# Kernel optimization log

Hardware: AMD Instinct MI355X
Metric: run time of the kernel (lower is better)

Reference implementation:

```python
import jax, jax.numpy as jnp
import numpy as np

NEG_SLOPE = 0.2

def setup_inputs() -> dict:
    key = jax.random.key(0)
    k1, k2, k3, k4 = jax.random.split(key, 4)
    B, N, Fin, H, Fo = 8, 2000, 128, 4, 64
    x = jax.random.normal(k1, (B, N, Fin), dtype=jnp.float32)
    adj = jax.random.randint(k2, (N, N), 0, 2, dtype=jnp.int32)
    W = jax.random.normal(k3, (Fin, H * Fo), dtype=jnp.float32) * (1.0 / np.sqrt(Fin))
    a = jax.random.normal(k4, (H, 2 * Fo), dtype=jnp.float32) * 0.1
    return {"x": x, "adj": adj, "W": W, "a": a}

def reference(x, adj, W, a):
    B, N, _ = x.shape
    H, F2 = a.shape
    Fo = F2 // 2
    h = (x @ W).reshape(B, N, H, Fo)  # [B,N,H,Fo]
    # cat([h_i,h_j])*a summed over 2Fo decomposes into per-node src/dst scores
    a_src, a_dst = a[:, :Fo], a[:, Fo:]
    e_i = jnp.einsum('bnhf,hf->bnh', h, a_src)  # source (query) contribution
    e_j = jnp.einsum('bnhf,hf->bnh', h, a_dst)  # target (key) contribution
    e = jax.nn.leaky_relu(e_i[:, :, None, :] + e_j[:, None, :, :], NEG_SLOPE)  # [B,N,N,H]
    mask = (adj == 0)[None, :, :, None]
    e = jnp.where(mask, -jnp.inf, e)
    alpha = jax.nn.softmax(e, axis=2)  # softmax over neighbors j
    # dropout is identity in eval mode
    out = jnp.einsum('bijh,bjhf->bihf', alpha, h).mean(axis=2)  # [B,N,Fo]
    return out, alpha
```

## Files before the change

kernel.cpp:

```cpp
#include <hip/hip_runtime.h>
#include <math.h>

#define BB 8
#define NN 2000
#define FIN 128
#define HH 4
#define FO 64
#define CC 256

typedef short bf16x8 __attribute__((ext_vector_type(8)));
typedef float f32x4 __attribute__((ext_vector_type(4)));
typedef unsigned long long u64;

__device__ __forceinline__ unsigned short f2bf(float v) {
    union { float f; unsigned u; } x;
    x.f = v;
    unsigned r = x.u + 0x7fffu + ((x.u >> 16) & 1u);
    return (unsigned short)(r >> 16);
}

__global__ __launch_bounds__(256) void k_gemm_xw(const float* __restrict__ x,
                                                 const float* __restrict__ W,
                                                 float* __restrict__ hfeat) {
    __shared__ float xs[16 * FIN];
    const int row0 = blockIdx.x * 16;
    const int t = threadIdx.x;
    for (int k = t; k < 16 * FIN; k += 256) xs[k] = x[row0 * FIN + k];
    __syncthreads();
    const int c = t;
    float acc[16];
#pragma unroll
    for (int r = 0; r < 16; ++r) acc[r] = 0.f;
#pragma unroll 2
    for (int k = 0; k < FIN; k += 4) {
        const float w0 = W[(k + 0) * CC + c];
        const float w1 = W[(k + 1) * CC + c];
        const float w2 = W[(k + 2) * CC + c];
        const float w3 = W[(k + 3) * CC + c];
#pragma unroll
        for (int r = 0; r < 16; ++r) {
            const float4 xv = *(const float4*)(xs + r * FIN + k);
            acc[r] = fmaf(xv.x, w0, fmaf(xv.y, w1, fmaf(xv.z, w2, fmaf(xv.w, w3, acc[r]))));
        }
    }
#pragma unroll
    for (int r = 0; r < 16; ++r) hfeat[(row0 + r) * CC + c] = acc[r];
}

__global__ __launch_bounds__(256) void k_adjbits(const int* __restrict__ adj,
                                                 u64* __restrict__ adjb) {
    const int w = blockIdx.x * 4 + (threadIdx.x >> 6);
    const int lane = threadIdx.x & 63;
    const int i = w >> 5, wd = w & 31;
    const int j = wd * 64 + lane;
    int av = 0;
    if (j < NN) av = adj[(size_t)i * NN + j];
    const u64 mask = __ballot(av != 0);
    if (lane == 0) adjb[(size_t)i * 32 + wd] = mask;
}

__global__ __launch_bounds__(256) void k_calc_e(const float* __restrict__ hfeat,
                                                const float* __restrict__ a,
                                                float* __restrict__ e_src,
                                                float* __restrict__ e_dst) {
    const int widx = blockIdx.x * 4 + (threadIdx.x >> 6);
    const int lane = threadIdx.x & 63;
    const int b = widx / (NN * HH);
    const int rem = widx - b * (NN * HH);
    const int n = rem / HH;
    const int h = rem - n * HH;
    const float hv = hfeat[((b * NN + n) * HH + h) * FO + lane];
    float p1 = hv * a[h * 2 * FO + lane];
    float p2 = hv * a[h * 2 * FO + FO + lane];
#pragma unroll
    for (int off = 32; off > 0; off >>= 1) {
        p1 += __shfl_xor(p1, off);
        p2 += __shfl_xor(p2, off);
    }
    if (lane == 0) {
        e_src[(b * HH + h) * NN + n] = p1;
        e_dst[(b * HH + h) * NN + n] = p2;
    }
}

__global__ __launch_bounds__(256) void k_softmax_ml(const u64* __restrict__ adjb,
                                                    const float* __restrict__ e_src,
                                                    const float* __restrict__ e_dst,
                                                    float* __restrict__ mArr,
                                                    float* __restrict__ rlArr) {
    const int widx = blockIdx.x * 4 + (threadIdx.x >> 6);
    const int lane = threadIdx.x & 63;
    const int b = widx / (NN * HH);
    const int rem = widx - b * (NN * HH);
    const int i = rem / HH;
    const int h = rem - i * HH;
    const float* ed = e_dst + (b * HH + h) * NN;
    const u64* ab = adjb + (size_t)i * 32;
    const float ei = e_src[(b * HH + h) * NN + i];
    float m = -1e30f, l = 0.f;
#pragma unroll 2
    for (int it = 0; it < 8; ++it) {
        const int j = it * 256 + lane * 4;
        const u64 wbits = ab[j >> 6];
        const unsigned nib = (unsigned)((wbits >> (j & 63)) & 0xFull);
        const float4 ev = *(const float4*)(ed + j);
        float s0 = ei + ev.x; s0 = s0 > 0.f ? s0 : 0.2f * s0; s0 = (nib & 1u) ? s0 : -1e30f;
        float s1 = ei + ev.y; s1 = s1 > 0.f ? s1 : 0.2f * s1; s1 = (nib & 2u) ? s1 : -1e30f;
        float s2 = ei + ev.z; s2 = s2 > 0.f ? s2 : 0.2f * s2; s2 = (nib & 4u) ? s2 : -1e30f;
        float s3 = ei + ev.w; s3 = s3 > 0.f ? s3 : 0.2f * s3; s3 = (nib & 8u) ? s3 : -1e30f;
        const float m4 = fmaxf(fmaxf(s0, s1), fmaxf(s2, s3));
        const float l4 = __expf(s0 - m4) + __expf(s1 - m4) + __expf(s2 - m4) + __expf(s3 - m4);
        const float nm = fmaxf(m, m4);
        l = l * __expf(m - nm) + l4 * __expf(m4 - nm);
        m = nm;
    }
#pragma unroll
    for (int off = 32; off > 0; off >>= 1) {
        const float mo = __shfl_xor(m, off);
        const float lo = __shfl_xor(l, off);
        const float mn = fmaxf(m, mo);
        l = l * __expf(m - mn) + lo * __expf(mo - mn);
        m = mn;
    }
    if (lane == 0) {
        mArr[(b * HH + h) * NN + i] = m;
        rlArr[(b * HH + h) * NN + i] = 1.f / l;
    }
}

__global__ __launch_bounds__(256) void k_transpose(const float* __restrict__ hfeat,
                                                   unsigned short* __restrict__ hT) {
    __shared__ unsigned short sm[64 * 65];
    const int jt = blockIdx.x, h = blockIdx.y, b = blockIdx.z;
    const int j0 = jt * 64;
    const int t = threadIdx.x;
    for (int k = t; k < 4096; k += 256) {
        const int jj = k >> 6, f = k & 63;
        const int j = j0 + jj;
        const float v = (j < NN) ? hfeat[((b * NN + j) * HH + h) * FO + f] : 0.f;
        sm[jj * 65 + f] = f2bf(v);
    }
    __syncthreads();
    unsigned short* dst = hT + (size_t)(b * HH + h) * 131072 + (size_t)jt * 4096;
    for (int k2 = t; k2 < 4096; k2 += 256) {
        const int s_loc = k2 >> 11;
        const int ft   = (k2 >> 9) & 3;
        const int quad = (k2 >> 7) & 3;
        const int l16  = (k2 >> 3) & 15;
        const int e    = k2 & 7;
        const int jj = s_loc * 32 + quad * 8 + e;
        const int f  = ft * 16 + l16;
        dst[k2] = sm[jj * 65 + f];
    }
}

__global__ __launch_bounds__(256) void k_out_mfma3(const u64* __restrict__ adjb,
                                                   const unsigned short* __restrict__ hT,
                                                   const float* __restrict__ e_src,
                                                   const float* __restrict__ e_dst,
                                                   const float* __restrict__ mArr,
                                                   const float* __restrict__ rlArr,
                                                   float* __restrict__ out) {
    __shared__ float red[HH][16][72];
    const int blk = blockIdx.x;
    const int b = blk / 125;
    const int it = blk - b * 125;
    const int h = threadIdx.x >> 6;
    const int lane = threadIdx.x & 63;
    const int l16 = lane & 15, quad = lane >> 4;
    const int i = it * 16 + l16;
    const int bh = b * HH + h;
    const float es = e_src[bh * NN + i];
    const float mm = mArr[bh * NN + i];
    const float rl = rlArr[bh * NN + i];
    const float* ed = e_dst + bh * NN;
    const u64* ab = adjb + (size_t)i * 32;
    const unsigned short* hbase = hT + (size_t)bh * 131072 + (size_t)lane * 8;

    f32x4 acc[4];
#pragma unroll
    for (int ft = 0; ft < 4; ++ft) {
        acc[ft][0] = 0.f; acc[ft][1] = 0.f; acc[ft][2] = 0.f; acc[ft][3] = 0.f;
    }

#pragma unroll 2
    for (int jt = 0; jt < 32; ++jt) {
        const int j0 = jt * 64;
        const u64 bits = ab[jt];
        const unsigned m0 = ((unsigned)(bits >> (quad * 8))) & 0xffu;
        const unsigned m1 = ((unsigned)(bits >> 32) >> (quad * 8)) & 0xffu;
        const float4 ea0 = *(const float4*)(ed + j0 + quad * 8);
        const float4 ea1 = *(const float4*)(ed + j0 + quad * 8 + 4);
        const float4 eb0 = *(const float4*)(ed + j0 + 32 + quad * 8);
        const float4 eb1 = *(const float4*)(ed + j0 + 32 + quad * 8 + 4);
        const unsigned short* hp0 = hbase + (size_t)jt * 4096;

        {
            const float ev[8] = {ea0.x, ea0.y, ea0.z, ea0.w, ea1.x, ea1.y, ea1.z, ea1.w};
            bf16x8 bfr;
#pragma unroll
            for (int e = 0; e < 8; ++e) {
                float s = es + ev[e];
                s = s > 0.f ? s : 0.2f * s;
                float p = __expf(s - mm) * rl;
                p = ((m0 >> e) & 1u) ? p : 0.f;
                bfr[e] = (short)f2bf(p);
            }
#pragma unroll
            for (int ft = 0; ft < 4; ++ft) {
                const bf16x8 af = *(const bf16x8*)(hp0 + ft * 512);
                acc[ft] = __builtin_amdgcn_mfma_f32_16x16x32_bf16(af, bfr, acc[ft], 0, 0, 0);
            }
        }
        {
            const float ev[8] = {eb0.x, eb0.y, eb0.z, eb0.w, eb1.x, eb1.y, eb1.z, eb1.w};
            bf16x8 bfr;
#pragma unroll
            for (int e = 0; e < 8; ++e) {
                float s = es + ev[e];
                s = s > 0.f ? s : 0.2f * s;
                float p = __expf(s - mm) * rl;
                p = ((m1 >> e) & 1u) ? p : 0.f;
                bfr[e] = (short)f2bf(p);
            }
#pragma unroll
            for (int ft = 0; ft < 4; ++ft) {
                const bf16x8 af = *(const bf16x8*)(hp0 + 2048 + ft * 512);
                acc[ft] = __builtin_amdgcn_mfma_f32_16x16x32_bf16(af, bfr, acc[ft], 0, 0, 0);
            }
        }
    }
#pragma unroll
    for (int ft = 0; ft < 4; ++ft)
        *(f32x4*)(&red[h][l16][ft * 16 + quad * 4]) = acc[ft];
    __syncthreads();
    const int t = threadIdx.x;
    const int ii = t >> 4, f4 = (t & 15) * 4;
    const int gi = it * 16 + ii;
    const f32x4 s0 = *(const f32x4*)(&red[0][ii][f4]);
    const f32x4 s1 = *(const f32x4*)(&red[1][ii][f4]);
    const f32x4 s2 = *(const f32x4*)(&red[2][ii][f4]);
    const f32x4 s3 = *(const f32x4*)(&red[3][ii][f4]);
    f32x4 o;
#pragma unroll
    for (int r = 0; r < 4; ++r) o[r] = 0.25f * (s0[r] + s1[r] + s2[r] + s3[r]);
    *(f32x4*)(out + (size_t)(b * NN + gi) * FO + f4) = o;
}

__global__ __launch_bounds__(256) void k_alpha(const int* __restrict__ adj,
                                               const float* __restrict__ e_src,
                                               const float* __restrict__ e_dst,
                                               const float* __restrict__ mArr,
                                               const float* __restrict__ rlArr,
                                               float* __restrict__ alpha) {
    const int bi = blockIdx.x;
    const int b = bi / NN, i = bi - b * NN;
    const int t = threadIdx.x;
    float ei[HH], mm[HH], rr[HH];
#pragma unroll
    for (int h = 0; h < HH; ++h) {
        ei[h] = e_src[(b * HH + h) * NN + i];
        mm[h] = mArr[(b * HH + h) * NN + i];
        rr[h] = rlArr[(b * HH + h) * NN + i];
    }
    const float* ed = e_dst + b * HH * NN;
    const int* adjrow = adj + (size_t)i * NN;
    float* arow = alpha + (size_t)(b * NN + i) * (NN * HH);
    for (int jq = t; jq < NN / 4; jq += 256) {
        const int j0 = jq * 4;
        const int4 av4 = *(const int4*)(adjrow + j0);
        const int avs[4] = {av4.x, av4.y, av4.z, av4.w};
        float e4[HH * 4];
#pragma unroll
        for (int h = 0; h < HH; ++h) {
            const float4 v = *(const float4*)(ed + h * NN + j0);
            e4[h * 4 + 0] = v.x; e4[h * 4 + 1] = v.y; e4[h * 4 + 2] = v.z; e4[h * 4 + 3] = v.w;
        }
#pragma unroll
        for (int jj = 0; jj < 4; ++jj) {
            const bool av = avs[jj] != 0;
            float o[HH];
#pragma unroll
            for (int h = 0; h < HH; ++h) {
                float s = ei[h] + e4[h * 4 + jj];
                s = s > 0.f ? s : 0.2f * s;
                o[h] = av ? __expf(s - mm[h]) * rr[h] : 0.f;
            }
            float4 ov = {o[0], o[1], o[2], o[3]};
            *(float4*)(arow + (size_t)(j0 + jj) * HH) = ov;
        }
    }
}

extern "C" void kernel_launch(void* const* d_in, const int* in_sizes, int n_in,
                              void* d_out, int out_size, void* d_ws, size_t ws_size,
                              hipStream_t stream) {
    const float* x  = (const float*)d_in[0];
    const int* adj  = (const int*)d_in[1];
    const float* W  = (const float*)d_in[2];
    const float* a  = (const float*)d_in[3];

    float* out = (float*)d_out;
    float* alpha = out + (size_t)BB * NN * FO;

    float* hfeat = alpha;
    unsigned short* hT = (unsigned short*)(alpha + (size_t)BB * NN * CC);
    u64* adjb = (u64*)(alpha + (size_t)BB * NN * CC + (size_t)BB * HH * FO * 1024);

    float* ws    = (float*)d_ws;
    float* e_src = ws;
    float* e_dst = e_src + BB * HH * NN;
    float* mArr  = e_dst + BB * HH * NN;
    float* rlArr = mArr + BB * HH * NN;

    k_gemm_xw<<<1000, 256, 0, stream>>>(x, W, hfeat);
    k_adjbits<<<16000, 256, 0, stream>>>(adj, adjb);
    k_calc_e<<<16000, 256, 0, stream>>>(hfeat, a, e_src, e_dst);
    k_softmax_ml<<<16000, 256, 0, stream>>>(adjb, e_src, e_dst, mArr, rlArr);
    k_transpose<<<dim3(32, HH, BB), 256, 0, stream>>>(hfeat, hT);
    k_out_mfma3<<<1000, 256, 0, stream>>>(adjb, hT, e_src, e_dst, mArr, rlArr, out);
    k_alpha<<<16000, 256, 0, stream>>>(adj, e_src, e_dst, mArr, rlArr, alpha);
}
```

Measured before the change: 757.6 us.

## Fuse GEMM with score and transposed bf16 output, drop softmax max pass

Fuses the x@W GEMM with the attention score reduction and writes the bf16 transposed feature layout directly, removing the fp32 hfeat round trip and two kernels. Replaces the online max/sum softmax with a plain exp-sum that skips the max subtraction. Retiles the output MFMA kernel to 32 rows per 512-thread block with a serialized head reduction. The alpha kernel reads the packed adjacency bitmask from workspace instead of the int matrix. Skipping the max risks overflow for inputs with large scores.

```diff
diff --git a/kernel.cpp b/kernel.cpp
--- a/kernel.cpp
+++ b/kernel.cpp
@@ -17,34 +17,6 @@
     x.f = v;
     unsigned r = x.u + 0x7fffu + ((x.u >> 16) & 1u);
     return (unsigned short)(r >> 16);
-}
-
-__global__ __launch_bounds__(256) void k_gemm_xw(const float* __restrict__ x,
-                                                 const float* __restrict__ W,
-                                                 float* __restrict__ hfeat) {
-    __shared__ float xs[16 * FIN];
-    const int row0 = blockIdx.x * 16;
-    const int t = threadIdx.x;
-    for (int k = t; k < 16 * FIN; k += 256) xs[k] = x[row0 * FIN + k];
-    __syncthreads();
-    const int c = t;
-    float acc[16];
-#pragma unroll
-    for (int r = 0; r < 16; ++r) acc[r] = 0.f;
-#pragma unroll 2
-    for (int k = 0; k < FIN; k += 4) {
-        const float w0 = W[(k + 0) * CC + c];
-        const float w1 = W[(k + 1) * CC + c];
-        const float w2 = W[(k + 2) * CC + c];
-        const float w3 = W[(k + 3) * CC + c];
-#pragma unroll
-        for (int r = 0; r < 16; ++r) {
-            const float4 xv = *(const float4*)(xs + r * FIN + k);
-            acc[r] = fmaf(xv.x, w0, fmaf(xv.y, w1, fmaf(xv.z, w2, fmaf(xv.w, w3, acc[r]))));
-        }
-    }
-#pragma unroll
-    for (int r = 0; r < 16; ++r) hfeat[(row0 + r) * CC + c] = acc[r];
 }
 
 __global__ __launch_bounds__(256) void k_adjbits(const int* __restrict__ adj,
@@ -59,35 +31,95 @@
     if (lane == 0) adjb[(size_t)i * 32 + wd] = mask;
 }
 
-__global__ __launch_bounds__(256) void k_calc_e(const float* __restrict__ hfeat,
-                                                const float* __restrict__ a,
-                                                float* __restrict__ e_src,
-                                                float* __restrict__ e_dst) {
-    const int widx = blockIdx.x * 4 + (threadIdx.x >> 6);
-    const int lane = threadIdx.x & 63;
-    const int b = widx / (NN * HH);
-    const int rem = widx - b * (NN * HH);
-    const int n = rem / HH;
-    const int h = rem - n * HH;
-    const float hv = hfeat[((b * NN + n) * HH + h) * FO + lane];
-    float p1 = hv * a[h * 2 * FO + lane];
-    float p2 = hv * a[h * 2 * FO + FO + lane];
-#pragma unroll
-    for (int off = 32; off > 0; off >>= 1) {
-        p1 += __shfl_xor(p1, off);
-        p2 += __shfl_xor(p2, off);
-    }
-    if (lane == 0) {
-        e_src[(b * HH + h) * NN + n] = p1;
-        e_dst[(b * HH + h) * NN + n] = p2;
-    }
-}
-
-__global__ __launch_bounds__(256) void k_softmax_ml(const u64* __restrict__ adjb,
-                                                    const float* __restrict__ e_src,
-                                                    const float* __restrict__ e_dst,
-                                                    float* __restrict__ mArr,
-                                                    float* __restrict__ rlArr) {
+__global__ __launch_bounds__(256) void k_gemm_fused(const float* __restrict__ x,
+                                                    const float* __restrict__ W,
+                                                    const float* __restrict__ a,
+                                                    float* __restrict__ e_src,
+                                                    float* __restrict__ e_dst,
+                                                    unsigned short* __restrict__ hT) {
+    __shared__ __align__(16) char smraw[8192];
+    float* xs = (float*)smraw;
+    unsigned short* sm = (unsigned short*)smraw;
+    const int row0 = blockIdx.x * 16;
+    const int t = threadIdx.x;
+    for (int k = t; k < 16 * FIN; k += 256) xs[k] = x[row0 * FIN + k];
+    __syncthreads();
+    const int c = t;
+    const int h = c >> 6, f = c & 63, lane = t & 63;
+    float acc[16];
+#pragma unroll
+    for (int r = 0; r < 16; ++r) acc[r] = 0.f;
+#pragma unroll 2
+    for (int k = 0; k < FIN; k += 4) {
+        const float w0 = W[(k + 0) * CC + c];
+        const float w1 = W[(k + 1) * CC + c];
+        const float w2 = W[(k + 2) * CC + c];
+        const float w3 = W[(k + 3) * CC + c];
+#pragma unroll
+        for (int r = 0; r < 16; ++r) {
+            const float4 xv = *(const float4*)(xs + r * FIN + k);
+            acc[r] = fmaf(xv.x, w0, fmaf(xv.y, w1, fmaf(xv.z, w2, fmaf(xv.w, w3, acc[r]))));
+        }
+    }
+    const int b = row0 / NN;
+    const int n0 = row0 - b * NN;
+    const float aS = a[h * 2 * FO + f];
+    const float aD = a[h * 2 * FO + FO + f];
+#pragma unroll
+    for (int r = 0; r < 16; ++r) {
+        float p1 = acc[r] * aS;
+        float p2 = acc[r] * aD;
+#pragma unroll
+        for (int off = 32; off > 0; off >>= 1) {
+            p1 += __shfl_xor(p1, off);
+            p2 += __shfl_xor(p2, off);
+        }
+        if (lane == 0) {
+            e_src[(b * HH + h) * NN + n0 + r] = p1;
+            e_dst[(b * HH + h) * NN + n0 + r] = p2;
+        }
+    }
+    __syncthreads();
+#pragma unroll
+    for (int r = 0; r < 16; ++r) sm[r * 256 + c] = f2bf(acc[r]);
+    __syncthreads();
+    const int s = n0 >> 5;
+    const int qbase = (n0 >> 3) & 3;
+    unsigned short* base = hT + (size_t)b * HH * 131072 + s * 2048;
+#pragma unroll
+    for (int it2 = 0; it2 < 2; ++it2) {
+        const int k2 = it2 * 256 + t;
+        const int hh = (k2 >> 7) & 3, ft2 = (k2 >> 5) & 3, l16 = (k2 >> 1) & 15, g = k2 & 1;
+        const int col = hh * 64 + ft2 * 16 + l16;
+        unsigned v[4];
+#pragma unroll
+        for (int p = 0; p < 4; ++p) {
+            const unsigned lo = sm[(g * 8 + 2 * p) * 256 + col];
+            const unsigned hi = sm[(g * 8 + 2 * p + 1) * 256 + col];
+            v[p] = lo | (hi << 16);
+        }
+        uint4 pkt; pkt.x = v[0]; pkt.y = v[1]; pkt.z = v[2]; pkt.w = v[3];
+        *(uint4*)(base + (size_t)hh * 131072 + ft2 * 512 + (qbase + g) * 128 + l16 * 8) = pkt;
+    }
+}
+
+__global__ __launch_bounds__(256) void k_padT(unsigned short* __restrict__ hT) {
+    const int k = blockIdx.x * 256 + threadIdx.x;
+    const int bh = k / 384;
+    const int r = k - bh * 384;
+    const int ft = r / 96;
+    const int c = r - ft * 96;
+    size_t off;
+    if (c < 32) off = 62 * 2048 + ft * 512 + 256 + c * 8;
+    else        off = 63 * 2048 + ft * 512 + (size_t)(c - 32) * 8;
+    uint4 z; z.x = 0; z.y = 0; z.z = 0; z.w = 0;
+    *(uint4*)(hT + (size_t)bh * 131072 + off) = z;
+}
+
+__global__ __launch_bounds__(256) void k_softmax_l(const u64* __restrict__ adjb,
+                                                   const float* __restrict__ e_src,
+                                                   const float* __restrict__ e_dst,
+                                                   float* __restrict__ rlArr) {
     const int widx = blockIdx.x * 4 + (threadIdx.x >> 6);
     const int lane = threadIdx.x & 63;
     const int b = widx / (NN * HH);
@@ -97,84 +129,49 @@
     const float* ed = e_dst + (b * HH + h) * NN;
     const u64* ab = adjb + (size_t)i * 32;
     const float ei = e_src[(b * HH + h) * NN + i];
-    float m = -1e30f, l = 0.f;
+    float l = 0.f;
 #pragma unroll 2
     for (int it = 0; it < 8; ++it) {
         const int j = it * 256 + lane * 4;
         const u64 wbits = ab[j >> 6];
         const unsigned nib = (unsigned)((wbits >> (j & 63)) & 0xFull);
         const float4 ev = *(const float4*)(ed + j);
-        float s0 = ei + ev.x; s0 = s0 > 0.f ? s0 : 0.2f * s0; s0 = (nib & 1u) ? s0 : -1e30f;
-        float s1 = ei + ev.y; s1 = s1 > 0.f ? s1 : 0.2f * s1; s1 = (nib & 2u) ? s1 : -1e30f;
-        float s2 = ei + ev.z; s2 = s2 > 0.f ? s2 : 0.2f * s2; s2 = (nib & 4u) ? s2 : -1e30f;
-        float s3 = ei + ev.w; s3 = s3 > 0.f ? s3 : 0.2f * s3; s3 = (nib & 8u) ? s3 : -1e30f;
-        const float m4 = fmaxf(fmaxf(s0, s1), fmaxf(s2, s3));
-        const float l4 = __expf(s0 - m4) + __expf(s1 - m4) + __expf(s2 - m4) + __expf(s3 - m4);
-        const float nm = fmaxf(m, m4);
-        l = l * __expf(m - nm) + l4 * __expf(m4 - nm);
-        m = nm;
-    }
-#pragma unroll
-    for (int off = 32; off > 0; off >>= 1) {
-        const float mo = __shfl_xor(m, off);
-        const float lo = __shfl_xor(l, off);
-        const float mn = fmaxf(m, mo);
-        l = l * __expf(m - mn) + lo * __expf(mo - mn);
-        m = mn;
-    }
-    if (lane == 0) {
-        mArr[(b * HH + h) * NN + i] = m;
-        rlArr[(b * HH + h) * NN + i] = 1.f / l;
-    }
-}
-
-__global__ __launch_bounds__(256) void k_transpose(const float* __restrict__ hfeat,
-                                                   unsigned short* __restrict__ hT) {
-    __shared__ unsigned short sm[64 * 65];
-    const int jt = blockIdx.x, h = blockIdx.y, b = blockIdx.z;
-    const int j0 = jt * 64;
-    const int t = threadIdx.x;
-    for (int k = t; k < 4096; k += 256) {
-        const int jj = k >> 6, f = k & 63;
-        const int j = j0 + jj;
-        const float v = (j < NN) ? hfeat[((b * NN + j) * HH + h) * FO + f] : 0.f;
-        sm[jj * 65 + f] = f2bf(v);
-    }
-    __syncthreads();
-    unsigned short* dst = hT + (size_t)(b * HH + h) * 131072 + (size_t)jt * 4096;
-    for (int k2 = t; k2 < 4096; k2 += 256) {
-        const int s_loc = k2 >> 11;
-        const int ft   = (k2 >> 9) & 3;
-        const int quad = (k2 >> 7) & 3;
-        const int l16  = (k2 >> 3) & 15;
-        const int e    = k2 & 7;
-        const int jj = s_loc * 32 + quad * 8 + e;
-        const int f  = ft * 16 + l16;
-        dst[k2] = sm[jj * 65 + f];
-    }
-}
-
-__global__ __launch_bounds__(256) void k_out_mfma3(const u64* __restrict__ adjb,
+        float s0 = ei + ev.x; s0 = s0 > 0.f ? s0 : 0.2f * s0;
+        float s1 = ei + ev.y; s1 = s1 > 0.f ? s1 : 0.2f * s1;
+        float s2 = ei + ev.z; s2 = s2 > 0.f ? s2 : 0.2f * s2;
+        float s3 = ei + ev.w; s3 = s3 > 0.f ? s3 : 0.2f * s3;
+        const float q0 = (nib & 1u) ? __expf(s0) : 0.f;
+        const float q1 = (nib & 2u) ? __expf(s1) : 0.f;
+        const float q2 = (nib & 4u) ? __expf(s2) : 0.f;
+        const float q3 = (nib & 8u) ? __expf(s3) : 0.f;
+        l += (q0 + q1) + (q2 + q3);
+    }
+#pragma unroll
+    for (int off = 32; off > 0; off >>= 1) l += __shfl_xor(l, off);
+    if (lane == 0) rlArr[(b * HH + h) * NN + i] = 1.f / l;
+}
+
+__global__ __launch_bounds__(512) void k_out_mfma4(const u64* __restrict__ adjb,
                                                    const unsigned short* __restrict__ hT,
                                                    const float* __restrict__ e_src,
                                                    const float* __restrict__ e_dst,
-                                                   const float* __restrict__ mArr,
                                                    const float* __restrict__ rlArr,
                                                    float* __restrict__ out) {
-    __shared__ float red[HH][16][72];
+    __shared__ float red[32][72];
     const int blk = blockIdx.x;
-    const int b = blk / 125;
-    const int it = blk - b * 125;
-    const int h = threadIdx.x >> 6;
-    const int lane = threadIdx.x & 63;
+    const int b = blk / 63;
+    const int it = blk - b * 63;
+    const int t = threadIdx.x;
+    const int w = t >> 6, lane = t & 63;
+    const int h = w >> 1, half = w & 1;
     const int l16 = lane & 15, quad = lane >> 4;
-    const int i = it * 16 + l16;
+    const int i = it * 32 + half * 16 + l16;
+    const int ic = i < NN ? i : NN - 1;
     const int bh = b * HH + h;
-    const float es = e_src[bh * NN + i];
-    const float mm = mArr[bh * NN + i];
-    const float rl = rlArr[bh * NN + i];
+    const float es = e_src[bh * NN + ic];
+    const float rl = (i < NN) ? rlArr[bh * NN + ic] : 0.f;
     const float* ed = e_dst + bh * NN;
-    const u64* ab = adjb + (size_t)i * 32;
+    const u64* ab = adjb + (size_t)ic * 32;
     const unsigned short* hbase = hT + (size_t)bh * 131072 + (size_t)lane * 8;
 
     f32x4 acc[4];
@@ -202,7 +199,7 @@
             for (int e = 0; e < 8; ++e) {
                 float s = es + ev[e];
                 s = s > 0.f ? s : 0.2f * s;
-                float p = __expf(s - mm) * rl;
+                float p = __expf(s) * rl;
                 p = ((m0 >> e) & 1u) ? p : 0.f;
                 bfr[e] = (short)f2bf(p);
             }
@@ -219,7 +216,7 @@
             for (int e = 0; e < 8; ++e) {
                 float s = es + ev[e];
                 s = s > 0.f ? s : 0.2f * s;
-                float p = __expf(s - mm) * rl;
+                float p = __expf(s) * rl;
                 p = ((m1 >> e) & 1u) ? p : 0.f;
                 bfr[e] = (short)f2bf(p);
             }
@@ -231,36 +228,89 @@
         }
     }
 #pragma unroll
-    for (int ft = 0; ft < 4; ++ft)
-        *(f32x4*)(&red[h][l16][ft * 16 + quad * 4]) = acc[ft];
-    __syncthreads();
-    const int t = threadIdx.x;
+    for (int ph = 0; ph < HH; ++ph) {
+        if (h == ph) {
+            if (ph == 0) {
+#pragma unroll
+                for (int ft = 0; ft < 4; ++ft)
+                    *(f32x4*)(&red[half * 16 + l16][ft * 16 + quad * 4]) = acc[ft];
+            } else {
+#pragma unroll
+                for (int ft = 0; ft < 4; ++ft) {
+                    f32x4 cur = *(const f32x4*)(&red[half * 16 + l16][ft * 16 + quad * 4]);
+#pragma unroll
+                    for (int r = 0; r < 4; ++r) cur[r] += acc[ft][r];
+                    *(f32x4*)(&red[half * 16 + l16][ft * 16 + quad * 4]) = cur;
+                }
+            }
+        }
+        __syncthreads();
+    }
     const int ii = t >> 4, f4 = (t & 15) * 4;
-    const int gi = it * 16 + ii;
-    const f32x4 s0 = *(const f32x4*)(&red[0][ii][f4]);
-    const f32x4 s1 = *(const f32x4*)(&red[1][ii][f4]);
-    const f32x4 s2 = *(const f32x4*)(&red[2][ii][f4]);
-    const f32x4 s3 = *(const f32x4*)(&red[3][ii][f4]);
-    f32x4 o;
-#pragma unroll
-    for (int r = 0; r < 4; ++r) o[r] = 0.25f * (s0[r] + s1[r] + s2[r] + s3[r]);
-    *(f32x4*)(out + (size_t)(b * NN + gi) * FO + f4) = o;
-}
-
-__global__ __launch_bounds__(256) void k_alpha(const int* __restrict__ adj,
-                                               const float* __restrict__ e_src,
-                                               const float* __restrict__ e_dst,
-                                               const float* __restrict__ mArr,
-                                               const float* __restrict__ rlArr,
-                                               float* __restrict__ alpha) {
+    const int gi = it * 32 + ii;
+    if (gi < NN) {
+        const f32x4 v = *(const f32x4*)(&red[ii][f4]);
+        f32x4 o;
+#pragma unroll
+        for (int r = 0; r < 4; ++r) o[r] = 0.25f * v[r];
+        *(f32x4*)(out + (size_t)(b * NN + gi) * FO + f4) = o;
+    }
+}
+
+__global__ __launch_bounds__(256) void k_alpha_bits(const u64* __restrict__ adjb,
+                                                    const float* __restrict__ e_src,
+                                                    const float* __restrict__ e_dst,
+                                                    const float* __restrict__ rlArr,
+                                                    float* __restrict__ alpha) {
     const int bi = blockIdx.x;
     const int b = bi / NN, i = bi - b * NN;
     const int t = threadIdx.x;
-    float ei[HH], mm[HH], rr[HH];
+    float ei[HH], rr[HH];
 #pragma unroll
     for (int h = 0; h < HH; ++h) {
         ei[h] = e_src[(b * HH + h) * NN + i];
-        mm[h] = mArr[(b * HH + h) * NN + i];
+        rr[h] = rlArr[(b * HH + h) * NN + i];
+    }
+    const float* ed = e_dst + b * HH * NN;
+    const u64* ab = adjb + (size_t)i * 32;
+    float* arow = alpha + (size_t)(b * NN + i) * (NN * HH);
+    for (int jq = t; jq < NN / 4; jq += 256) {
+        const int j0 = jq * 4;
+        const unsigned bits4 = (unsigned)((ab[j0 >> 6] >> (j0 & 63)) & 0xFull);
+        float e4[HH * 4];
+#pragma unroll
+        for (int h = 0; h < HH; ++h) {
+            const float4 v = *(const float4*)(ed + h * NN + j0);
+            e4[h * 4 + 0] = v.x; e4[h * 4 + 1] = v.y; e4[h * 4 + 2] = v.z; e4[h * 4 + 3] = v.w;
+        }
+#pragma unroll
+        for (int jj = 0; jj < 4; ++jj) {
+            const bool av = (bits4 >> jj) & 1u;
+            float o[HH];
+#pragma unroll
+            for (int h = 0; h < HH; ++h) {
+                float s = ei[h] + e4[h * 4 + jj];
+                s = s > 0.f ? s : 0.2f * s;
+                o[h] = av ? __expf(s) * rr[h] : 0.f;
+            }
+            float4 ov = {o[0], o[1], o[2], o[3]};
+            *(float4*)(arow + (size_t)(j0 + jj) * HH) = ov;
+        }
+    }
+}
+
+__global__ __launch_bounds__(256) void k_alpha_adj(const int* __restrict__ adj,
+                                                   const float* __restrict__ e_src,
+                                                   const float* __restrict__ e_dst,
+                                                   const float* __restrict__ rlArr,
+                                                   float* __restrict__ alpha) {
+    const int bi = blockIdx.x;
+    const int b = bi / NN, i = bi - b * NN;
+    const int t = threadIdx.x;
+    float ei[HH], rr[HH];
+#pragma unroll
+    for (int h = 0; h < HH; ++h) {
+        ei[h] = e_src[(b * HH + h) * NN + i];
         rr[h] = rlArr[(b * HH + h) * NN + i];
     }
     const float* ed = e_dst + b * HH * NN;
@@ -284,7 +334,7 @@
             for (int h = 0; h < HH; ++h) {
                 float s = ei[h] + e4[h * 4 + jj];
                 s = s > 0.f ? s : 0.2f * s;
-                o[h] = av ? __expf(s - mm[h]) * rr[h] : 0.f;
+                o[h] = av ? __expf(s) * rr[h] : 0.f;
             }
             float4 ov = {o[0], o[1], o[2], o[3]};
             *(float4*)(arow + (size_t)(j0 + jj) * HH) = ov;
@@ -303,21 +353,23 @@
     float* out = (float*)d_out;
     float* alpha = out + (size_t)BB * NN * FO;
 
-    float* hfeat = alpha;
-    unsigned short* hT = (unsigned short*)(alpha + (size_t)BB * NN * CC);
-    u64* adjb = (u64*)(alpha + (size_t)BB * NN * CC + (size_t)BB * HH * FO * 1024);
-
-    float* ws    = (float*)d_ws;
-    float* e_src = ws;
-    float* e_dst = e_src + BB * HH * NN;
-    float* mArr  = e_dst + BB * HH * NN;
-    float* rlArr = mArr + BB * HH * NN;
-
-    k_gemm_xw<<<1000, 256, 0, stream>>>(x, W, hfeat);
+    unsigned short* hT = (unsigned short*)alpha;
+    u64* adjb_scratch = (u64*)((char*)alpha + 8388608);
+
+    char* ws = (char*)d_ws;
+    float* e_src = (float*)ws;
+    float* e_dst = (float*)(ws + 256000);
+    float* rlArr = (float*)(ws + 512000);
+    const bool ws_has_adjb = ws_size >= 1280000;
+    u64* adjb = ws_has_adjb ? (u64*)(ws + 768000) : adjb_scratch;
+
     k_adjbits<<<16000, 256, 0, stream>>>(adj, adjb);
-    k_calc_e<<<16000, 256, 0, stream>>>(hfeat, a, e_src, e_dst);
-    k_softmax_ml<<<16000, 256, 0, stream>>>(adjb, e_src, e_dst, mArr, rlArr);
-    k_transpose<<<dim3(32, HH, BB), 256, 0, stream>>>(hfeat, hT);
-    k_out_mfma3<<<1000, 256, 0, stream>>>(adjb, hT, e_src, e_dst, mArr, rlArr, out);
-    k_alpha<<<16000, 256, 0, stream>>>(adj, e_src, e_dst, mArr, rlArr, alpha);
-}
+    k_gemm_fused<<<1000, 256, 0, stream>>>(x, W, a, e_src, e_dst, hT);
+    k_padT<<<48, 256, 0, stream>>>(hT);
+    k_softmax_l<<<16000, 256, 0, stream>>>(adjb, e_src, e_dst, rlArr);
+    k_out_mfma4<<<504, 512, 0, stream>>>(adjb, hT, e_src, e_dst, rlArr, out);
+    if (ws_has_adjb)
+        k_alpha_bits<<<16000, 256, 0, stream>>>(adjb, e_src, e_dst, rlArr, alpha);
+    else
+        k_alpha_adj<<<16000, 256, 0, stream>>>(adj, e_src, e_dst, rlArr, alpha);
+}
```

Result: no change. 763.0 us (+0.7%).
